# Kernel tuning notes

Hardware: AMD Instinct MI355X
Metric: run time of the kernel (lower is better)

The kernel has to match this reference:

```python
import jax, jax.numpy as jnp
import numpy as np

S, B, H = 512, 32, 1024      # seq, batch, hidden_size
L = 4096                      # total spans (flattened ragged labels)
D = 1024                      # label_size (feature dim)
V = 32000                     # vocab size


def setup_inputs() -> dict:
    key = jax.random.key(0)
    ks = jax.random.split(key, 10)
    hidden = jax.random.normal(ks[0], (S, B, H), dtype=jnp.float32)
    span_bid = jax.random.randint(ks[1], (L,), 0, B)
    span_begin = jax.random.randint(ks[2], (L,), 0, S)
    span_end_m1 = jax.random.randint(ks[3], (L,), 0, S)  # (end - 1) index
    tags = jax.random.randint(ks[4], (L,), 0, V)
    # hidden2feature: Linear(2H -> D) with bias, Tanh
    W1 = jax.random.normal(ks[5], (D, 2 * H), dtype=jnp.float32) * (1.0 / np.sqrt(2 * H))
    b1 = jnp.zeros((D,), dtype=jnp.float32)
    # SoftmaxLoss h2o: Linear(D -> V, bias=False)
    Wout = jax.random.normal(ks[6], (V, D), dtype=jnp.float32) * (1.0 / np.sqrt(D))
    # discard probs from synthetic frequency counts
    counts = jax.random.uniform(ks[7], (V,), minval=1e-5, maxval=1.0)
    freqs = counts / counts.sum()
    discard_probs = jnp.clip(1.0 - jnp.sqrt(1e-4 / freqs), 0.0, None)
    return {"hidden": hidden, "W1": W1, "b1": b1, "Wout": Wout,
            "discard_probs": discard_probs, "span_bid": span_bid,
            "span_begin": span_begin, "span_end_m1": span_end_m1, "tags": tags}


def reference(hidden, W1, b1, Wout, discard_probs, span_bid, span_begin, span_end_m1, tags):
    # gather span endpoint embeddings: [L, H] each
    emb_b = hidden[span_begin, span_bid]
    emb_e = hidden[span_end_m1, span_bid]
    span_emb = jnp.concatenate([emb_b, emb_e], axis=-1)          # [L, 2H]
    feat = jnp.tanh(span_emb @ W1.T + b1)                        # [L, D]
    logits = feat @ Wout.T                                       # [L, V]
    logp = jax.nn.log_softmax(logits, axis=-1)
    nll = -jnp.take_along_axis(logp, tags[:, None], axis=-1)[:, 0]  # [L]
    scaled = 1.0 - discard_probs[tags]
    n_tags = tags.shape[0]
    return jnp.sum(nll * scaled) / (n_tags + 1e-5)
```

## Files before the change

kernel.cpp:

```cpp
#include <hip/hip_runtime.h>
#include <hip/hip_bf16.h>

#define LSPANS 4096
#define BB 32
#define HH 1024
#define DD 1024
#define VV 32000
#define K1 2048
#define NT2 125

typedef unsigned short u16;
typedef __attribute__((ext_vector_type(8))) short bf16x8v;
typedef __attribute__((ext_vector_type(4))) float f32x4v;

__device__ __forceinline__ u16 f2bf(float x) {
  union { float f; unsigned u; } v; v.f = x;
  unsigned r = (v.u >> 16) & 1u;
  return (u16)((v.u + 0x7fffu + r) >> 16);
}

__global__ void cvt_kernel(const float* __restrict__ in, u16* __restrict__ out, int n4) {
  int i = blockIdx.x * blockDim.x + threadIdx.x;
  int stride = gridDim.x * blockDim.x;
  for (; i < n4; i += stride) {
    float4 v = ((const float4*)in)[i];
    ushort4 o;
    o.x = f2bf(v.x); o.y = f2bf(v.y); o.z = f2bf(v.z); o.w = f2bf(v.w);
    ((ushort4*)out)[i] = o;
  }
}

__global__ void gather_kernel(const float* __restrict__ hidden,
                              const int* __restrict__ bid,
                              const int* __restrict__ sb,
                              const int* __restrict__ se,
                              u16* __restrict__ out) {
  int l = blockIdx.x;
  int t = threadIdx.x;
  int b  = bid[l];
  const float* p0 = hidden + ((size_t)sb[l] * BB + b) * HH;
  const float* p1 = hidden + ((size_t)se[l] * BB + b) * HH;
  u16* dst = out + (size_t)l * K1;
  float4 v0 = ((const float4*)p0)[t];
  float4 v1 = ((const float4*)p1)[t];
  ushort4 o0; o0.x = f2bf(v0.x); o0.y = f2bf(v0.y); o0.z = f2bf(v0.z); o0.w = f2bf(v0.w);
  ushort4 o1; o1.x = f2bf(v1.x); o1.y = f2bf(v1.y); o1.z = f2bf(v1.z); o1.w = f2bf(v1.w);
  ((ushort4*)dst)[t]          = o0;
  ((ushort4*)(dst + HH))[t]   = o1;
}

__launch_bounds__(256, 2)
__global__ void gemm128_kernel(const u16* __restrict__ A, const u16* __restrict__ B,
                               int Ntot, const float* __restrict__ bias,
                               u16* __restrict__ feat_out) {
  __shared__ __align__(16) u16 As[128 * 64];
  __shared__ __align__(16) u16 Bs[128 * 64];

  const int tid  = threadIdx.x;
  const int lane = tid & 63;
  const int w    = tid >> 6;
  const int wm   = w & 1;
  const int wn   = w >> 1;
  const int q    = lane >> 4;
  const int lm   = lane & 15;
  const int mBase = blockIdx.x * 128;
  const int nBase = blockIdx.y * 128;

  f32x4v acc[4][4];
#pragma unroll
  for (int i = 0; i < 4; ++i)
#pragma unroll
    for (int j = 0; j < 4; ++j) acc[i][j] = (f32x4v){0.f, 0.f, 0.f, 0.f};

  const int srow = w * 32 + (lane >> 3);
  const int scol = ((lane & 7) ^ (lane >> 3)) * 8;
  const u16* Ag = A + (size_t)(mBase + srow) * K1 + scol;
  const u16* Bg = B + (size_t)(nBase + srow) * K1 + scol;

  for (int k0 = 0; k0 < K1; k0 += 64) {
#pragma unroll
    for (int c = 0; c < 4; ++c) {
      __builtin_amdgcn_global_load_lds(
          (const __attribute__((address_space(1))) void*)(Ag + k0 + (size_t)c * 8 * K1),
          (__attribute__((address_space(3))) void*)(As + (w * 32 + c * 8) * 64), 16, 0, 0);
    }
#pragma unroll
    for (int c = 0; c < 4; ++c) {
      __builtin_amdgcn_global_load_lds(
          (const __attribute__((address_space(1))) void*)(Bg + k0 + (size_t)c * 8 * K1),
          (__attribute__((address_space(3))) void*)(Bs + (w * 32 + c * 8) * 64), 16, 0, 0);
    }
    __syncthreads();
#pragma unroll
    for (int kk = 0; kk < 64; kk += 32) {
      bf16x8v af[4], bfr[4];
      const int sw = lm & 7;
#pragma unroll
      for (int i = 0; i < 4; ++i) {
        int row = wm * 64 + i * 16 + lm;
        int kch = (kk >> 3) + q;
        af[i] = *(const bf16x8v*)(As + row * 64 + ((kch ^ sw) << 3));
      }
#pragma unroll
      for (int j = 0; j < 4; ++j) {
        int row = wn * 64 + j * 16 + lm;
        int kch = (kk >> 3) + q;
        bfr[j] = *(const bf16x8v*)(Bs + row * 64 + ((kch ^ sw) << 3));
      }
#pragma unroll
      for (int i = 0; i < 4; ++i)
#pragma unroll
        for (int j = 0; j < 4; ++j)
          acc[i][j] = __builtin_amdgcn_mfma_f32_16x16x32_bf16(af[i], bfr[j], acc[i][j], 0, 0, 0);
    }
    __syncthreads();
  }

  float bj[4];
#pragma unroll
  for (int j = 0; j < 4; ++j) bj[j] = bias[nBase + wn * 64 + j * 16 + lm];
#pragma unroll
  for (int i = 0; i < 4; ++i)
#pragma unroll
    for (int j = 0; j < 4; ++j)
#pragma unroll
      for (int r = 0; r < 4; ++r) {
        int tr = wm * 64 + i * 16 + q * 4 + r;
        int tc = wn * 64 + j * 16 + lm;
        float v = tanhf(acc[i][j][r] + bj[j]);
        feat_out[(size_t)(mBase + tr) * Ntot + nBase + tc] = f2bf(v);
      }
}

#define STAGE256(pp, k0) do {                                                       \
  _Pragma("unroll")                                                                 \
  for (int c = 0; c < 4; ++c)                                                       \
    __builtin_amdgcn_global_load_lds(                                               \
        (const __attribute__((address_space(1))) void*)(Ag + (k0) + (size_t)c * 8 * DD), \
        (__attribute__((address_space(3))) void*)(&As[pp][(w * 32 + c * 8) * 64]), 16, 0, 0); \
  _Pragma("unroll")                                                                 \
  for (int c = 0; c < 4; ++c)                                                       \
    __builtin_amdgcn_global_load_lds(                                               \
        (const __attribute__((address_space(1))) void*)(Bg + (k0) + (size_t)c * 8 * DD), \
        (__attribute__((address_space(3))) void*)(&Bs[pp][(w * 32 + c * 8) * 64]), 16, 0, 0); \
} while (0)

__launch_bounds__(512, 2)
__global__ void gemm256_kernel(const u16* __restrict__ A, const u16* __restrict__ B,
                               const int* __restrict__ tags,
                               float* __restrict__ pmax, float* __restrict__ psum,
                               float* __restrict__ ltag) {
  __shared__ __align__(16) u16 As[2][256 * 64];
  __shared__ __align__(16) u16 Bs[2][256 * 64];
  __shared__ float rmax[4][256];
  __shared__ float rsum[4][256];
  __shared__ int   stags[256];

  const int tid  = threadIdx.x;
  const int lane = tid & 63;
  const int w    = tid >> 6;
  const int wm   = w >> 2;
  const int wn   = w & 3;
  const int q    = lane >> 4;
  const int lm   = lane & 15;
  const int sw   = lm & 7;
  const int mBase = blockIdx.x * 256;
  const int nBase = blockIdx.y * 256;

  if (tid < 256) stags[tid] = tags[mBase + tid];

  f32x4v acc[8][4];
#pragma unroll
  for (int i = 0; i < 8; ++i)
#pragma unroll
    for (int j = 0; j < 4; ++j) acc[i][j] = (f32x4v){0.f, 0.f, 0.f, 0.f};

  const int srow = w * 32 + (lane >> 3);
  const int scol = ((lane & 7) ^ (lane >> 3)) * 8;
  const u16* Ag = A + (size_t)(mBase + srow) * DD + scol;
  const u16* Bg = B + (size_t)(nBase + srow) * DD + scol;

  const int aoff = (wm * 128 + lm) * 64;
  const int boff = (wn * 64 + lm) * 64;
  const int c0 = (q ^ sw) << 3;
  const int c1 = ((q + 4) ^ sw) << 3;

  STAGE256(0, 0);
  STAGE256(1, 64);
  asm volatile("s_waitcnt vmcnt(8)" ::: "memory");
  __builtin_amdgcn_s_barrier();
  __builtin_amdgcn_sched_barrier(0);

  const int NT = DD / 64;
#pragma unroll 2
  for (int t = 0; t < NT; ++t) {
    const int p = t & 1;
    const u16* Asp = &As[p][0];
    const u16* Bsp = &Bs[p][0];
    bf16x8v a0[4], a1[4], b0[4], b1[4];

#pragma unroll
    for (int i = 0; i < 4; ++i) a0[i] = *(const bf16x8v*)(Asp + aoff + i * 1024 + c0);
#pragma unroll
    for (int j = 0; j < 4; ++j) b0[j] = *(const bf16x8v*)(Bsp + boff + j * 1024 + c0);
    __builtin_amdgcn_s_barrier();
    asm volatile("s_waitcnt lgkmcnt(0)" ::: "memory");
    __builtin_amdgcn_sched_barrier(0);
    __builtin_amdgcn_s_setprio(1);
#pragma unroll
    for (int i = 0; i < 4; ++i)
#pragma unroll
      for (int j = 0; j < 4; ++j)
        acc[i][j] = __builtin_amdgcn_mfma_f32_16x16x32_bf16(a0[i], b0[j], acc[i][j], 0, 0, 0);
    __builtin_amdgcn_s_setprio(0);
    __builtin_amdgcn_s_barrier();

#pragma unroll
    for (int i = 0; i < 4; ++i) a1[i] = *(const bf16x8v*)(Asp + aoff + (i + 4) * 1024 + c0);
#pragma unroll
    for (int j = 0; j < 4; ++j) b1[j] = *(const bf16x8v*)(Bsp + boff + j * 1024 + c1);
    __builtin_amdgcn_s_barrier();
    asm volatile("s_waitcnt lgkmcnt(0)" ::: "memory");
    __builtin_amdgcn_sched_barrier(0);
    __builtin_amdgcn_s_setprio(1);
#pragma unroll
    for (int i = 0; i < 4; ++i)
#pragma unroll
      for (int j = 0; j < 4; ++j)
        acc[4 + i][j] = __builtin_amdgcn_mfma_f32_16x16x32_bf16(a1[i], b0[j], acc[4 + i][j], 0, 0, 0);
    __builtin_amdgcn_s_setprio(0);
    __builtin_amdgcn_s_barrier();

#pragma unroll
    for (int i = 0; i < 4; ++i) a0[i] = *(const bf16x8v*)(Asp + aoff + i * 1024 + c1);
#pragma unroll
    for (int i = 0; i < 4; ++i) a1[i] = *(const bf16x8v*)(Asp + aoff + (i + 4) * 1024 + c1);
    __builtin_amdgcn_s_barrier();
    asm volatile("s_waitcnt lgkmcnt(0)" ::: "memory");
    __builtin_amdgcn_sched_barrier(0);
    __builtin_amdgcn_s_setprio(1);
#pragma unroll
    for (int i = 0; i < 4; ++i)
#pragma unroll
      for (int j = 0; j < 4; ++j)
        acc[i][j] = __builtin_amdgcn_mfma_f32_16x16x32_bf16(a0[i], b1[j], acc[i][j], 0, 0, 0);
    __builtin_amdgcn_s_setprio(0);
    __builtin_amdgcn_s_barrier();

    if (t + 2 < NT) STAGE256(p, (t + 2) * 64);
    __builtin_amdgcn_s_barrier();
    __builtin_amdgcn_s_setprio(1);
#pragma unroll
    for (int i = 0; i < 4; ++i)
#pragma unroll
      for (int j = 0; j < 4; ++j)
        acc[4 + i][j] = __builtin_amdgcn_mfma_f32_16x16x32_bf16(a1[i], b1[j], acc[4 + i][j], 0, 0, 0);
    __builtin_amdgcn_s_setprio(0);
    if (t + 2 < NT) {
      asm volatile("s_waitcnt vmcnt(8)" ::: "memory");
    } else if (t + 1 < NT) {
      asm volatile("s_waitcnt vmcnt(0)" ::: "memory");
    }
    __builtin_amdgcn_s_barrier();
  }

#pragma unroll
  for (int i = 0; i < 8; ++i)
#pragma unroll
    for (int r = 0; r < 4; ++r) {
      float m = fmaxf(fmaxf(acc[i][0][r], acc[i][1][r]),
                      fmaxf(acc[i][2][r], acc[i][3][r]));
#pragma unroll
      for (int off = 1; off < 16; off <<= 1) m = fmaxf(m, __shfl_xor(m, off, 64));
      if (lm == 0) rmax[wn][wm * 128 + i * 16 + q * 4 + r] = m;
    }
  __syncthreads();
#pragma unroll
  for (int i = 0; i < 8; ++i)
#pragma unroll
    for (int r = 0; r < 4; ++r) {
      int tr = wm * 128 + i * 16 + q * 4 + r;
      float M = fmaxf(fmaxf(rmax[0][tr], rmax[1][tr]),
                      fmaxf(rmax[2][tr], rmax[3][tr]));
      float s = __expf(acc[i][0][r] - M) + __expf(acc[i][1][r] - M) +
                __expf(acc[i][2][r] - M) + __expf(acc[i][3][r] - M);
#pragma unroll
      for (int off = 1; off < 16; off <<= 1) s += __shfl_xor(s, off, 64);
      if (lm == 0) rsum[wn][tr] = s;
    }
  __syncthreads();
  if (tid < 256) {
    float M = fmaxf(fmaxf(rmax[0][tid], rmax[1][tid]),
                    fmaxf(rmax[2][tid], rmax[3][tid]));
    float S = rsum[0][tid] + rsum[1][tid] + rsum[2][tid] + rsum[3][tid];
    pmax[(size_t)blockIdx.y * LSPANS + mBase + tid] = M;
    psum[(size_t)blockIdx.y * LSPANS + mBase + tid] = S;
  }
#pragma unroll
  for (int i = 0; i < 8; ++i)
#pragma unroll
    for (int r = 0; r < 4; ++r) {
      int tr = wm * 128 + i * 16 + q * 4 + r;
      int tg = stags[tr];
#pragma unroll
      for (int j = 0; j < 4; ++j) {
        int gc = nBase + wn * 64 + j * 16 + lm;
        if (tg == gc) ltag[mBase + tr] = acc[i][j][r];
      }
    }
}

__global__ void finalize_kernel(const float* __restrict__ pmax, const float* __restrict__ psum,
                                const float* __restrict__ ltag, const int* __restrict__ tags,
                                const float* __restrict__ dprob, float* __restrict__ out) {
  int l = blockIdx.x * blockDim.x + threadIdx.x;
  const float* pm = pmax + l;
  const float* ps = psum + l;
  float M = -1e30f;
  for (int t = 0; t < NT2; ++t) M = fmaxf(M, pm[(size_t)t * LSPANS]);
  float S = 0.f;
  for (int t = 0; t < NT2; ++t) S += ps[(size_t)t * LSPANS] * __expf(pm[(size_t)t * LSPANS] - M);
  float nll = M + logf(S) - ltag[l];
  float wgt = 1.0f - dprob[tags[l]];
  float val = nll * wgt * (1.0f / (4096.0f + 1e-5f));
  __shared__ float red[4];
#pragma unroll
  for (int off = 32; off; off >>= 1) val += __shfl_down(val, off, 64);
  if ((threadIdx.x & 63) == 0) red[threadIdx.x >> 6] = val;
  __syncthreads();
  if (threadIdx.x == 0) atomicAdd(out, red[0] + red[1] + red[2] + red[3]);
}

extern "C" void kernel_launch(void* const* d_in, const int* in_sizes, int n_in,
                              void* d_out, int out_size, void* d_ws, size_t ws_size,
                              hipStream_t stream) {
  const float* hidden = (const float*)d_in[0];
  const float* W1     = (const float*)d_in[1];
  const float* b1     = (const float*)d_in[2];
  const float* Wout   = (const float*)d_in[3];
  const float* dprob  = (const float*)d_in[4];
  const int*   bid    = (const int*)d_in[5];
  const int*   sb     = (const int*)d_in[6];
  const int*   se     = (const int*)d_in[7];
  const int*   tags   = (const int*)d_in[8];
  float* out = (float*)d_out;

  char* ws = (char*)d_ws;
  u16* A1    = (u16*)ws;                 ws += (size_t)LSPANS * K1 * 2;
  u16* W1b   = (u16*)ws;                 ws += (size_t)DD * K1 * 2;
  u16* Woutb = (u16*)ws;                 ws += (size_t)VV * DD * 2;
  u16* feat  = (u16*)ws;                 ws += (size_t)LSPANS * DD * 2;
  float* pmax = (float*)ws;              ws += (size_t)NT2 * LSPANS * 4;
  float* psum = (float*)ws;              ws += (size_t)NT2 * LSPANS * 4;
  float* ltag = (float*)ws;              ws += (size_t)LSPANS * 4;

  hipMemsetAsync(d_out, 0, sizeof(float), stream);

  {
    int n4 = DD * K1 / 4;
    cvt_kernel<<<(n4 + 255) / 256, 256, 0, stream>>>(W1, W1b, n4);
  }
  {
    int n4 = VV * DD / 4;
    cvt_kernel<<<(n4 + 255) / 256, 256, 0, stream>>>(Wout, Woutb, n4);
  }
  gather_kernel<<<LSPANS, 256, 0, stream>>>(hidden, bid, sb, se, A1);

  gemm128_kernel<<<dim3(LSPANS / 128, DD / 128), 256, 0, stream>>>(
      A1, W1b, DD, b1, feat);

  gemm256_kernel<<<dim3(LSPANS / 256, VV / 256), 512, 0, stream>>>(
      feat, Woutb, tags, pmax, psum, ltag);

  finalize_kernel<<<LSPANS / 256, 256, 0, stream>>>(pmax, psum, ltag, tags, dprob, out);
}
```

Measured before the change: 673.9 us.

## Software-pipeline LDS fragment loads across MFMA groups and remap block order

Restructures the main GEMM loop so that LDS fragment reads for the next MFMA group are issued while the current group runs. Partial lgkmcnt waits replace full drains, most per-phase barriers are removed, and the first fragments of the next k-tile are prefetched before the last MFMA group. It also remaps the linear block index so consecutive workgroups are spread across the vocab dimension in strides, which changes L2 reuse. Tag values are now read straight from global memory instead of being staged in shared memory. The changes add register pressure and rely on the fine-grained waitcnt counts being correct.

```diff
diff --git a/kernel.cpp b/kernel.cpp
--- a/kernel.cpp
+++ b/kernel.cpp
@@ -145,6 +145,17 @@
         (__attribute__((address_space(3))) void*)(&Bs[pp][(w * 32 + c * 8) * 64]), 16, 0, 0); \
 } while (0)
 
+#define MFMA_G(base, av, bv) do {                                                   \
+  _Pragma("unroll")                                                                 \
+  for (int i_ = 0; i_ < 4; ++i_)                                                    \
+    _Pragma("unroll")                                                               \
+    for (int j_ = 0; j_ < 4; ++j_)                                                  \
+      acc[(base) + i_][j_] = __builtin_amdgcn_mfma_f32_16x16x32_bf16(               \
+          av[i_], bv[j_], acc[(base) + i_][j_], 0, 0, 0);                           \
+} while (0)
+
+#define SB __builtin_amdgcn_sched_barrier(0)
+
 __launch_bounds__(512, 2)
 __global__ void gemm256_kernel(const u16* __restrict__ A, const u16* __restrict__ B,
                                const int* __restrict__ tags,
@@ -154,7 +165,6 @@
   __shared__ __align__(16) u16 Bs[2][256 * 64];
   __shared__ float rmax[4][256];
   __shared__ float rsum[4][256];
-  __shared__ int   stags[256];
 
   const int tid  = threadIdx.x;
   const int lane = tid & 63;
@@ -163,11 +173,13 @@
   const int wn   = w & 3;
   const int q    = lane >> 4;
   const int lm   = lane & 15;
-  const int sw   = lm & 7;
-  const int mBase = blockIdx.x * 256;
-  const int nBase = blockIdx.y * 256;
-
-  if (tid < 256) stags[tid] = tags[mBase + tid];
+  const int sw   = lm & 15 & 7;
+  const int lin = blockIdx.y * 16 + blockIdx.x;
+  const int nl  = (lin & 7) * 250 + (lin >> 3);
+  const int bx  = nl & 15;
+  const int by  = nl >> 4;
+  const int mBase = bx * 256;
+  const int nBase = by * 256;
 
   f32x4v acc[8][4];
 #pragma unroll
@@ -189,7 +201,16 @@
   STAGE256(1, 64);
   asm volatile("s_waitcnt vmcnt(8)" ::: "memory");
   __builtin_amdgcn_s_barrier();
-  __builtin_amdgcn_sched_barrier(0);
+  SB;
+  bf16x8v a0[4], b0[4], a1[4];
+#pragma unroll
+  for (int i = 0; i < 4; ++i) a0[i] = *(const bf16x8v*)(&As[0][0] + aoff + i * 1024 + c0);
+#pragma unroll
+  for (int j = 0; j < 4; ++j) b0[j] = *(const bf16x8v*)(&Bs[0][0] + boff + j * 1024 + c0);
+  SB;
+#pragma unroll
+  for (int i = 0; i < 4; ++i) a1[i] = *(const bf16x8v*)(&As[0][0] + aoff + (i + 4) * 1024 + c0);
+  SB;
 
   const int NT = DD / 64;
 #pragma unroll 2
@@ -197,71 +218,64 @@
     const int p = t & 1;
     const u16* Asp = &As[p][0];
     const u16* Bsp = &Bs[p][0];
-    bf16x8v a0[4], a1[4], b0[4], b1[4];
-
-#pragma unroll
-    for (int i = 0; i < 4; ++i) a0[i] = *(const bf16x8v*)(Asp + aoff + i * 1024 + c0);
-#pragma unroll
-    for (int j = 0; j < 4; ++j) b0[j] = *(const bf16x8v*)(Bsp + boff + j * 1024 + c0);
+    const u16* Asn = &As[p ^ 1][0];
+    const u16* Bsn = &Bs[p ^ 1][0];
+
+    asm volatile("s_waitcnt lgkmcnt(4)" ::: "memory");
+    SB;
+    __builtin_amdgcn_s_setprio(1);
+    MFMA_G(0, a0, b0);
+    __builtin_amdgcn_s_setprio(0);
+    bf16x8v a2[4], b1[4];
+#pragma unroll
+    for (int i = 0; i < 4; ++i) a2[i] = *(const bf16x8v*)(Asp + aoff + i * 1024 + c1);
+#pragma unroll
+    for (int j = 0; j < 4; ++j) b1[j] = *(const bf16x8v*)(Bsp + boff + j * 1024 + c1);
+    SB;
+
+    asm volatile("s_waitcnt lgkmcnt(8)" ::: "memory");
+    SB;
+    __builtin_amdgcn_s_setprio(1);
+    MFMA_G(4, a1, b0);
+    __builtin_amdgcn_s_setprio(0);
+    bf16x8v a3[4];
+#pragma unroll
+    for (int i = 0; i < 4; ++i) a3[i] = *(const bf16x8v*)(Asp + aoff + (i + 4) * 1024 + c1);
+    SB;
+
+    asm volatile("s_waitcnt lgkmcnt(4)" ::: "memory");
+    SB;
+    __builtin_amdgcn_s_setprio(1);
+    MFMA_G(0, a2, b1);
+    __builtin_amdgcn_s_setprio(0);
+
+    asm volatile("s_waitcnt lgkmcnt(0)" ::: "memory");
+    SB;
     __builtin_amdgcn_s_barrier();
-    asm volatile("s_waitcnt lgkmcnt(0)" ::: "memory");
-    __builtin_amdgcn_sched_barrier(0);
+    SB;
+    if (t + 2 < NT) STAGE256(p, (t + 2) * 64);
+    if (t + 1 < NT) {
+      if (t + 2 < NT) {
+        asm volatile("s_waitcnt vmcnt(8)" ::: "memory");
+      } else {
+        asm volatile("s_waitcnt vmcnt(0)" ::: "memory");
+      }
+      SB;
+      __builtin_amdgcn_s_barrier();
+      SB;
+#pragma unroll
+      for (int i = 0; i < 4; ++i) a0[i] = *(const bf16x8v*)(Asn + aoff + i * 1024 + c0);
+#pragma unroll
+      for (int j = 0; j < 4; ++j) b0[j] = *(const bf16x8v*)(Bsn + boff + j * 1024 + c0);
+      SB;
+#pragma unroll
+      for (int i = 0; i < 4; ++i) a1[i] = *(const bf16x8v*)(Asn + aoff + (i + 4) * 1024 + c0);
+      SB;
+    }
+
     __builtin_amdgcn_s_setprio(1);
-#pragma unroll
-    for (int i = 0; i < 4; ++i)
-#pragma unroll
-      for (int j = 0; j < 4; ++j)
-        acc[i][j] = __builtin_amdgcn_mfma_f32_16x16x32_bf16(a0[i], b0[j], acc[i][j], 0, 0, 0);
+    MFMA_G(4, a3, b1);
     __builtin_amdgcn_s_setprio(0);
-    __builtin_amdgcn_s_barrier();
-
-#pragma unroll
-    for (int i = 0; i < 4; ++i) a1[i] = *(const bf16x8v*)(Asp + aoff + (i + 4) * 1024 + c0);
-#pragma unroll
-    for (int j = 0; j < 4; ++j) b1[j] = *(const bf16x8v*)(Bsp + boff + j * 1024 + c1);
-    __builtin_amdgcn_s_barrier();
-    asm volatile("s_waitcnt lgkmcnt(0)" ::: "memory");
-    __builtin_amdgcn_sched_barrier(0);
-    __builtin_amdgcn_s_setprio(1);
-#pragma unroll
-    for (int i = 0; i < 4; ++i)
-#pragma unroll
-      for (int j = 0; j < 4; ++j)
-        acc[4 + i][j] = __builtin_amdgcn_mfma_f32_16x16x32_bf16(a1[i], b0[j], acc[4 + i][j], 0, 0, 0);
-    __builtin_amdgcn_s_setprio(0);
-    __builtin_amdgcn_s_barrier();
-
-#pragma unroll
-    for (int i = 0; i < 4; ++i) a0[i] = *(const bf16x8v*)(Asp + aoff + i * 1024 + c1);
-#pragma unroll
-    for (int i = 0; i < 4; ++i) a1[i] = *(const bf16x8v*)(Asp + aoff + (i + 4) * 1024 + c1);
-    __builtin_amdgcn_s_barrier();
-    asm volatile("s_waitcnt lgkmcnt(0)" ::: "memory");
-    __builtin_amdgcn_sched_barrier(0);
-    __builtin_amdgcn_s_setprio(1);
-#pragma unroll
-    for (int i = 0; i < 4; ++i)
-#pragma unroll
-      for (int j = 0; j < 4; ++j)
-        acc[i][j] = __builtin_amdgcn_mfma_f32_16x16x32_bf16(a0[i], b1[j], acc[i][j], 0, 0, 0);
-    __builtin_amdgcn_s_setprio(0);
-    __builtin_amdgcn_s_barrier();
-
-    if (t + 2 < NT) STAGE256(p, (t + 2) * 64);
-    __builtin_amdgcn_s_barrier();
-    __builtin_amdgcn_s_setprio(1);
-#pragma unroll
-    for (int i = 0; i < 4; ++i)
-#pragma unroll
-      for (int j = 0; j < 4; ++j)
-        acc[4 + i][j] = __builtin_amdgcn_mfma_f32_16x16x32_bf16(a1[i], b1[j], acc[4 + i][j], 0, 0, 0);
-    __builtin_amdgcn_s_setprio(0);
-    if (t + 2 < NT) {
-      asm volatile("s_waitcnt vmcnt(8)" ::: "memory");
-    } else if (t + 1 < NT) {
-      asm volatile("s_waitcnt vmcnt(0)" ::: "memory");
-    }
-    __builtin_amdgcn_s_barrier();
   }
 
 #pragma unroll
@@ -293,15 +307,15 @@
     float M = fmaxf(fmaxf(rmax[0][tid], rmax[1][tid]),
                     fmaxf(rmax[2][tid], rmax[3][tid]));
     float S = rsum[0][tid] + rsum[1][tid] + rsum[2][tid] + rsum[3][tid];
-    pmax[(size_t)blockIdx.y * LSPANS + mBase + tid] = M;
-    psum[(size_t)blockIdx.y * LSPANS + mBase + tid] = S;
+    pmax[(size_t)by * LSPANS + mBase + tid] = M;
+    psum[(size_t)by * LSPANS + mBase + tid] = S;
   }
 #pragma unroll
   for (int i = 0; i < 8; ++i)
 #pragma unroll
     for (int r = 0; r < 4; ++r) {
       int tr = wm * 128 + i * 16 + q * 4 + r;
-      int tg = stags[tr];
+      int tg = tags[mBase + tr];
 #pragma unroll
       for (int j = 0; j < 4; ++j) {
         int gc = nBase + wn * 64 + j * 16 + lm;
```

Measured after the change: 719.9 us. +6.8%, slower.
